# Kernel tuning notes

Measured on AMD Instinct MI355X. Metric: run time of the kernel, lower is better.

## Reference

```python
import jax, jax.numpy as jnp
import numpy as np

N = 16000        # nodes
E = 256000       # edges
D_IN = 1280      # input node features
HID = 256        # hidden dim (all hidden_dims equal; required by res_linear shapes)
HEADS = 8
C = HID // HEADS # 32 channels per head
G = 32           # graphs in the batch
O = 64           # output labels (GO terms)
NB = 2           # conv blocks = len(hidden_dims) - 1
EPS = 1e-5


def _bn(h, g, b):
    # eval-mode BatchNorm1d with running_mean=0, running_var=1 (init state)
    return h * (g / jnp.sqrt(1.0 + EPS)) + b


def _seg_softmax(logits, seg, num):
    # numerically-stable segment softmax (PyG softmax semantics)
    m = jax.ops.segment_max(logits, seg, num_segments=num)
    e = jnp.exp(logits - m[seg])
    s = jax.ops.segment_sum(e, seg, num_segments=num)
    return e / (s[seg] + 1e-16)


def setup_inputs() -> dict:
    key = jax.random.key(0)
    ks = jax.random.split(key, 16)
    w = lambda i, sh: jax.random.normal(ks[i], sh, jnp.float32) * 0.05
    return {
        "x": jax.random.normal(ks[0], (N, D_IN), jnp.float32),
        "edge_index": jax.random.randint(ks[1], (2, E), 0, N),
        "batch": jnp.sort(jax.random.randint(ks[2], (N,), 0, G)),
        # feature_proj: Linear -> ReLU -> BN
        "fp_W": w(3, (D_IN, HID)), "fp_b": jnp.zeros(HID),
        "fp_g": jnp.ones(HID), "fp_be": jnp.zeros(HID),
        # GATv2Conv per block: lin_l, lin_r, att, out-bias
        "gat_Wl": w(4, (NB, HID, HID)), "gat_bl": jnp.zeros((NB, HID)),
        "gat_Wr": w(5, (NB, HID, HID)), "gat_br": jnp.zeros((NB, HID)),
        "gat_att": w(6, (NB, HEADS, C)), "gat_bias": jnp.zeros((NB, HID)),
        # GINConv MLP: Linear -> ReLU -> BN
        "gin_W": w(7, (NB, HID, HID)), "gin_b": jnp.zeros((NB, HID)),
        "gin_g": jnp.ones((NB, HID)), "gin_be": jnp.zeros((NB, HID)),
        # PyG LayerNorm (graph mode) affine
        "ln_g": jnp.ones((NB, HID)), "ln_b": jnp.zeros((NB, HID)),
        # residual linears
        "res_W": w(8, (NB, HID, HID)), "res_b": jnp.zeros((NB, HID)),
        # GlobalAttention gate MLP
        "pool_W1": w(9, (HID, HID)), "pool_b1": jnp.zeros(HID),
        "pool_W2": w(10, (HID, 1)), "pool_b2": jnp.zeros(1),
        # O label heads (hierarchy=None -> just the MLP), stacked
        "head_W1": w(11, (O, HID, 256)), "head_b1": jnp.zeros((O, 256)),
        "head_g": jnp.ones((O, 256)), "head_be": jnp.zeros((O, 256)),
        "head_W2": w(12, (O, 256)), "head_b2": jnp.zeros(O),
    }


def reference(x, edge_index, batch, fp_W, fp_b, fp_g, fp_be,
              gat_Wl, gat_bl, gat_Wr, gat_br, gat_att, gat_bias,
              gin_W, gin_b, gin_g, gin_be, ln_g, ln_b, res_W, res_b,
              pool_W1, pool_b1, pool_W2, pool_b2,
              head_W1, head_b1, head_g, head_be, head_W2, head_b2):
    n = x.shape[0]
    # feature_proj (eval: dropout = identity)
    h = _bn(jax.nn.relu(x @ fp_W + fp_b), fp_g, fp_be)

    src0, dst0 = edge_index[0], edge_index[1]
    loop = jnp.arange(n)
    src = jnp.concatenate([src0, loop])  # GATv2 adds self-loops by default
    dst = jnp.concatenate([dst0, loop])

    for i in range(NB):
        # ---- GATv2Conv (no activation after, per original control flow) ----
        xl = (h @ gat_Wl[i] + gat_bl[i]).reshape(n, HEADS, C)
        xr = (h @ gat_Wr[i] + gat_br[i]).reshape(n, HEADS, C)
        msg = xl[src]                                   # [E', H, C]
        eact = jax.nn.leaky_relu(msg + xr[dst], 0.2)
        logit = jnp.einsum('ehc,hc->eh', eact, gat_att[i])
        alpha = _seg_softmax(logit, dst, n)             # [E', H]
        h = jax.ops.segment_sum(alpha[:, :, None] * msg, dst,
                                num_segments=n).reshape(n, HID) + gat_bias[i]
        # ---- GINConv: nn((1+0)*x + sum_neighbors), then leaky_relu ----
        agg = jax.ops.segment_sum(h[src0], dst0, num_segments=n)
        gin = _bn(jax.nn.relu((h + agg) @ gin_W[i] + gin_b[i]), gin_g[i], gin_be[i])
        h = jax.nn.leaky_relu(gin, 0.2)
        # ---- PyG LayerNorm (graph mode, batch=None: global mean/std) + residual ----
        mu = h.mean()
        sd = jnp.std(h)
        ln = (h - mu) / (sd + EPS) * ln_g[i] + ln_b[i]
        h = jax.nn.leaky_relu(ln + (h @ res_W[i] + res_b[i]), 0.2)

    # ---- GlobalAttention pooling ----
    gate = jnp.tanh(h @ pool_W1 + pool_b1) @ pool_W2 + pool_b2   # [N, 1]
    a = _seg_softmax(gate[:, 0], batch, G)
    emb = jax.ops.segment_sum(a[:, None] * h, batch, num_segments=G)  # [G, HID]

    # ---- O label heads (hierarchy None -> MLP only), vectorized ----
    z = jnp.einsum('bd,odh->boh', emb, head_W1) + head_b1[None]
    z = _bn(jax.nn.silu(z), head_g[None], head_be[None])
    out = jnp.einsum('boh,oh->bo', z, head_W2) + head_b2[None]
    return out[:, :, None]  # torch.stack(outputs, dim=1) -> [G, O, 1]
```

## Files before the change

### kernel.cpp

```cpp
#include <hip/hip_runtime.h>
#include <math.h>

#define N_NODES 16000
#define N_EDGES 256000
#define EPE (N_EDGES + N_NODES)
#define DIN 1280
#define HID 256
#define HEADS 8
#define CPH 32
#define NG 32
#define NO 64
#define EPSC 1e-5f
#define CAP 32
#define XPAD 264
#define SPAD 40

typedef __bf16 bf16;
typedef __attribute__((ext_vector_type(8))) __bf16 bf16x8;
typedef __attribute__((ext_vector_type(4))) float floatx4;

__device__ __forceinline__ float lrelu(float v) { return v > 0.f ? v : 0.2f * v; }
__device__ __forceinline__ float bflo(unsigned int u) { return __uint_as_float(u << 16); }
__device__ __forceinline__ float bfhi(unsigned int u) { return __uint_as_float(u & 0xffff0000u); }

__global__ void wconv_gen(const float* __restrict__ W, bf16* __restrict__ Wt, int K, int total) {
    int idx = blockIdx.x * 256 + threadIdx.x;
    if (idx >= total) return;
    int per = K * HID;
    int l = idx / per, rem = idx - l * per;
    int n = rem / K, k = rem - n * K;
    Wt[idx] = (bf16)W[(size_t)l * per + (size_t)k * HID + n];
}

__global__ void wconv_pair(const float* __restrict__ Wl, const float* __restrict__ Wr,
                           bf16* __restrict__ Wt) {
    int idx = blockIdx.x * 256 + threadIdx.x;
    int n = idx >> 8, k = idx & 255;
    float v = (n < 256) ? Wl[(size_t)k * HID + n] : Wr[(size_t)k * HID + (n - 256)];
    Wt[idx] = (bf16)v;
}

__global__ __launch_bounds__(256) void gemm64(
    const bf16* __restrict__ A, const bf16* __restrict__ Bt,
    const float* __restrict__ bias, const float* __restrict__ bias2,
    bf16* __restrict__ C, int K, int ldc, int mode,
    const float* __restrict__ g, const float* __restrict__ be)
{
    __shared__ __align__(16) bf16 As[2][64 * SPAD];
    __shared__ __align__(16) bf16 Bs[2][64 * SPAD];
    const int tid = threadIdx.x;
    const int bm = blockIdx.y * 64, bn = blockIdx.x * 64;
    const int w = tid >> 6, lane = tid & 63;
    const int wm = w * 16;
    const int lrow = lane & 15, lk8 = (lane >> 4) * 8;
    const int row = tid >> 2, k8 = (tid & 3) * 8;

    const bf16* gA = A + (size_t)(bm + row) * K + k8;
    const bf16* gB = Bt + (size_t)(bn + row) * K + k8;

    floatx4 acc[4];
#pragma unroll
    for (int j = 0; j < 4; j++) acc[j] = (floatx4){0.f, 0.f, 0.f, 0.f};

    const int nk = K >> 5;
    bf16x8 ra = *(const bf16x8*)gA;
    bf16x8 rb = *(const bf16x8*)gB;

    for (int it = 0; it < nk; ++it) {
        int p = it & 1;
        *(bf16x8*)&As[p][row * SPAD + k8] = ra;
        *(bf16x8*)&Bs[p][row * SPAD + k8] = rb;
        __syncthreads();
        if (it + 1 < nk) {
            ra = *(const bf16x8*)(gA + (it + 1) * 32);
            rb = *(const bf16x8*)(gB + (it + 1) * 32);
        }
        bf16x8 af = *(const bf16x8*)&As[p][(wm + lrow) * SPAD + lk8];
        bf16x8 bfr[4];
#pragma unroll
        for (int j = 0; j < 4; j++) bfr[j] = *(const bf16x8*)&Bs[p][(16 * j + lrow) * SPAD + lk8];
#pragma unroll
        for (int j = 0; j < 4; j++)
            acc[j] = __builtin_amdgcn_mfma_f32_16x16x32_bf16(af, bfr[j], acc[j], 0, 0, 0);
    }

    const float inv = rsqrtf(1.f + EPSC);
    const int row0 = bm + wm + (lane >> 4) * 4;
#pragma unroll
    for (int j = 0; j < 4; j++) {
        int col = bn + 16 * j + lrow;
        float bcol = (col < HID) ? bias[col] : bias2[col - HID];
        float gc = (mode >= 1) ? g[col] * inv : 0.f;
        float bec = (mode >= 1) ? be[col] : 0.f;
#pragma unroll
        for (int r = 0; r < 4; r++) {
            float z = acc[j][r] + bcol;
            if (mode >= 1) { z = fmaxf(z, 0.f); z = z * gc + bec; }
            if (mode == 2) z = lrelu(z);
            C[(size_t)(row0 + r) * ldc + col] = (bf16)z;
        }
    }
}

__global__ __launch_bounds__(256, 1) void gemm_f32A(
    const float* __restrict__ A, const bf16* __restrict__ Bt,
    const float* __restrict__ bias, bf16* __restrict__ C, int K,
    const float* __restrict__ g, const float* __restrict__ be)
{
    __shared__ __align__(16) bf16 As[2][128 * SPAD];
    __shared__ __align__(16) bf16 Bs[2][128 * SPAD];
    const int tid = threadIdx.x;
    const int bm = blockIdx.y * 128, bn = blockIdx.x * 128;
    const int w = tid >> 6, lane = tid & 63;
    const int wm = (w & 1) * 64, wn = (w >> 1) * 64;
    const int lrow = lane & 15, lk8 = (lane >> 4) * 8;

    floatx4 acc[4][4];
#pragma unroll
    for (int i = 0; i < 4; i++)
#pragma unroll
        for (int j = 0; j < 4; j++) acc[i][j] = (floatx4){0.f, 0.f, 0.f, 0.f};

    const int r2 = tid >> 1, c2 = tid & 1;
    const float* gA = A + (size_t)(bm + r2) * K + c2 * 16;
    const bf16* gB = Bt + (size_t)(bn + r2) * K + c2 * 16;
    bf16* sA = &As[0][r2 * SPAD + c2 * 16];
    bf16* sB = &Bs[0][r2 * SPAD + c2 * 16];

    const int nk = K >> 5;
    float4 a[4][4];
    bf16x8 b[4][2];
#pragma unroll
    for (int u = 0; u < 4; u++) {
        const float* pa = gA + u * 32;
        a[u][0] = *(const float4*)(pa + 0);
        a[u][1] = *(const float4*)(pa + 4);
        a[u][2] = *(const float4*)(pa + 8);
        a[u][3] = *(const float4*)(pa + 12);
        const bf16* pb = gB + u * 32;
        b[u][0] = *(const bf16x8*)(pb + 0);
        b[u][1] = *(const bf16x8*)(pb + 8);
    }

    for (int it0 = 0; it0 < nk; it0 += 4) {
#pragma unroll
        for (int u = 0; u < 4; u++) {
            const int it = it0 + u;
            const int p = u & 1;
            const int po = p * 128 * SPAD;
            bf16x8 h0, h1;
            h0[0] = (bf16)a[u][0].x; h0[1] = (bf16)a[u][0].y; h0[2] = (bf16)a[u][0].z; h0[3] = (bf16)a[u][0].w;
            h0[4] = (bf16)a[u][1].x; h0[5] = (bf16)a[u][1].y; h0[6] = (bf16)a[u][1].z; h0[7] = (bf16)a[u][1].w;
            h1[0] = (bf16)a[u][2].x; h1[1] = (bf16)a[u][2].y; h1[2] = (bf16)a[u][2].z; h1[3] = (bf16)a[u][2].w;
            h1[4] = (bf16)a[u][3].x; h1[5] = (bf16)a[u][3].y; h1[6] = (bf16)a[u][3].z; h1[7] = (bf16)a[u][3].w;
            *(bf16x8*)(sA + po + 0) = h0;
            *(bf16x8*)(sA + po + 8) = h1;
            *(bf16x8*)(sB + po + 0) = b[u][0];
            *(bf16x8*)(sB + po + 8) = b[u][1];
            __syncthreads();
            if (it + 4 < nk) {
                const float* pa = gA + (it + 4) * 32;
                a[u][0] = *(const float4*)(pa + 0);
                a[u][1] = *(const float4*)(pa + 4);
                a[u][2] = *(const float4*)(pa + 8);
                a[u][3] = *(const float4*)(pa + 12);
                const bf16* pb = gB + (it + 4) * 32;
                b[u][0] = *(const bf16x8*)(pb + 0);
                b[u][1] = *(const bf16x8*)(pb + 8);
            }
            bf16x8 af[4], bfr[4];
#pragma unroll
            for (int i = 0; i < 4; i++) af[i] = *(const bf16x8*)&As[p][(wm + 16 * i + lrow) * SPAD + lk8];
#pragma unroll
            for (int j = 0; j < 4; j++) bfr[j] = *(const bf16x8*)&Bs[p][(wn + 16 * j + lrow) * SPAD + lk8];
#pragma unroll
            for (int i = 0; i < 4; i++)
#pragma unroll
                for (int j = 0; j < 4; j++)
                    acc[i][j] = __builtin_amdgcn_mfma_f32_16x16x32_bf16(af[i], bfr[j], acc[i][j], 0, 0, 0);
        }
    }

    const float inv = rsqrtf(1.f + EPSC);
#pragma unroll
    for (int j = 0; j < 4; j++) {
        int col = bn + wn + 16 * j + lrow;
        float bcol = bias[col];
        float gc = g[col] * inv;
        float bec = be[col];
#pragma unroll
        for (int i = 0; i < 4; i++) {
            int row0 = bm + wm + 16 * i + (lane >> 4) * 4;
#pragma unroll
            for (int r = 0; r < 4; r++) {
                float z = fmaxf(acc[i][j][r] + bcol, 0.f) * gc + bec;
                C[(size_t)(row0 + r) * HID + col] = (bf16)z;
            }
        }
    }
}

__global__ void hist_kernel(const int* __restrict__ ei, int* __restrict__ cnt) {
    int e = blockIdx.x * 256 + threadIdx.x;
    if (e >= EPE) return;
    int d = (e < N_EDGES) ? ei[N_EDGES + e] : (e - N_EDGES);
    atomicAdd(&cnt[d], 1);
}

__global__ __launch_bounds__(1024) void scan_kernel(const int* __restrict__ cnt,
                                                    int* __restrict__ roff, int* __restrict__ cursor) {
    __shared__ int wsum[16];
    int t = threadIdx.x;
    int base = t * 16;
    int local[16]; int s = 0;
#pragma unroll
    for (int i = 0; i < 16; i++) {
        int idx = base + i;
        int v = (idx < N_NODES) ? cnt[idx] : 0;
        local[i] = s; s += v;
    }
    int lane = t & 63, wid = t >> 6;
    int incl = s;
    for (int o = 1; o < 64; o <<= 1) { int v = __shfl_up(incl, o); if (lane >= o) incl += v; }
    if (lane == 63) wsum[wid] = incl;
    __syncthreads();
    if (t == 0) { int a = 0; for (int k = 0; k < 16; k++) { int v = wsum[k]; wsum[k] = a; a += v; } }
    __syncthreads();
    int texcl = incl - s + wsum[wid];
#pragma unroll
    for (int i = 0; i < 16; i++) {
        int idx = base + i;
        if (idx < N_NODES) { int o = texcl + local[i]; roff[idx] = o; cursor[idx] = o; }
    }
    if (t == 1023) roff[N_NODES] = texcl + s;
}

__global__ void scatter_kernel(const int* __restrict__ ei, int* __restrict__ cursor,
                               int* __restrict__ esrc) {
    int e = blockIdx.x * 256 + threadIdx.x;
    if (e >= EPE) return;
    int s, d;
    if (e < N_EDGES) { s = ei[e]; d = ei[N_EDGES + e]; }
    else { s = d = e - N_EDGES; }
    int pos = atomicAdd(&cursor[d], 1);
    esrc[pos] = s;
}

__global__ __launch_bounds__(256) void gat_fused(
    const bf16* __restrict__ XLR, const int* __restrict__ roff, const int* __restrict__ esrc,
    const float* __restrict__ att, const float* __restrict__ gbias, bf16* __restrict__ out)
{
    const int d = blockIdx.x, t = threadIdx.x;
    const int beg = roff[d], deg = roff[d + 1] - beg;
    __shared__ __align__(16) bf16 xs[CAP][XPAD];
    __shared__ __align__(16) float4 xa4[8 * 16];
    __shared__ float llog[CAP * 8];
    __shared__ float m_s[8], s_s[8], resc[8];

    if (t < 128) {
        int hh = t >> 4, cc = t & 15;
        int c = hh * 32 + cc * 2;
        float xr0 = (float)XLR[(size_t)d * 512 + 256 + c];
        float xr1 = (float)XLR[(size_t)d * 512 + 256 + c + 1];
        xa4[hh * 16 + cc] = (float4){xr0, att[c], xr1, att[c + 1]};
    }
    if (t < 8) { m_s[t] = -INFINITY; s_s[t] = 0.f; }

    const int jj = t & 31;
    const int hh = t >> 5;
    const int g = t >> 5, l = t & 31;
    float acc = 0.f;

    for (int c0 = 0; c0 < deg; c0 += CAP) {
        int cn = min(CAP, deg - c0);
        __syncthreads();
        for (int r = g; r < cn; r += 8) {
            int s = esrc[beg + c0 + r];
            *(bf16x8*)(&xs[r][l * 8]) = *(const bf16x8*)(XLR + (size_t)s * 512 + l * 8);
        }
        __syncthreads();
        if (jj < cn) {
            float lg = 0.f;
#pragma unroll
            for (int cc = 0; cc < 16; cc++) {
                int ce = (cc + jj) & 15;
                unsigned int p = *(const unsigned int*)&xs[jj][hh * 32 + ce * 2];
                float4 xa = xa4[hh * 16 + ce];
                lg += lrelu(bflo(p) + xa.x) * xa.y + lrelu(bfhi(p) + xa.z) * xa.w;
            }
            llog[jj * 8 + hh] = lg;
        }
        __syncthreads();
        if (t < 64) {
            int h2 = t & 7, j0 = t >> 3;
            float mx = -INFINITY;
            for (int j = j0; j < cn; j += 8) mx = fmaxf(mx, llog[j * 8 + h2]);
            for (int o = 8; o < 64; o <<= 1) mx = fmaxf(mx, __shfl_xor(mx, o));
            float mo = m_s[h2];
            float mn = fmaxf(mo, mx);
            float ss = 0.f;
            for (int j = j0; j < cn; j += 8) {
                float e = __expf(llog[j * 8 + h2] - mn);
                llog[j * 8 + h2] = e;
                ss += e;
            }
            for (int o = 8; o < 64; o <<= 1) ss += __shfl_xor(ss, o);
            if (t < 8) {
                float r = __expf(mo - mn);
                resc[h2] = r;
                s_s[h2] = s_s[h2] * r + ss;
                m_s[h2] = mn;
            }
        }
        __syncthreads();
        acc *= resc[hh];
        for (int j = 0; j < cn; j++)
            acc += llog[j * 8 + hh] * (float)xs[j][t];
    }
    out[(size_t)d * HID + t] = (bf16)(gbias[t] + acc / (s_s[hh] + 1e-16f));
}

__global__ __launch_bounds__(256) void gin_gather(
    const unsigned int* __restrict__ hu, const int* __restrict__ roff,
    const int* __restrict__ esrc, unsigned int* __restrict__ uu)
{
    int d = blockIdx.x, t = threadIdx.x;
    int grp = t >> 7, c = t & 127;
    int beg = roff[d], end = roff[d + 1];
    float a0 = 0.f, a1 = 0.f;
    int p = beg + grp;
    while (p + 14 < end) {
        int s[8];
#pragma unroll
        for (int k = 0; k < 8; k++) s[k] = esrc[p + 2 * k];
        unsigned int v[8];
#pragma unroll
        for (int k = 0; k < 8; k++) v[k] = hu[(size_t)s[k] * 128 + c];
#pragma unroll
        for (int k = 0; k < 8; k++) { a0 += bflo(v[k]); a1 += bfhi(v[k]); }
        p += 16;
    }
    for (; p < end; p += 2) {
        unsigned int v = hu[(size_t)esrc[p] * 128 + c];
        a0 += bflo(v); a1 += bfhi(v);
    }
    __shared__ float plo[128], phi[128];
    if (grp) { plo[c] = a0; phi[c] = a1; }
    __syncthreads();
    if (!grp) {
        a0 += plo[c]; a1 += phi[c];
        bf16 b0 = (bf16)a0, b1 = (bf16)a1;
        unsigned int r = ((unsigned int)*(unsigned short*)&b0) |
                         (((unsigned int)*(unsigned short*)&b1) << 16);
        uu[(size_t)d * 128 + c] = r;
    }
}

__global__ void stats_kernel(const bf16* __restrict__ x, float2* __restrict__ part, int n8) {
    float s = 0.f, sq = 0.f;
    for (int i = blockIdx.x * blockDim.x + threadIdx.x; i < n8; i += gridDim.x * blockDim.x) {
        bf16x8 v = *(const bf16x8*)(x + (size_t)i * 8);
#pragma unroll
        for (int j = 0; j < 8; j++) { float f = (float)v[j]; s += f; sq += f * f; }
    }
    for (int o = 32; o > 0; o >>= 1) { s += __shfl_down(s, o); sq += __shfl_down(sq, o); }
    __shared__ float ls[4], lq[4];
    int wid = threadIdx.x >> 6, lane = threadIdx.x & 63;
    if (lane == 0) { ls[wid] = s; lq[wid] = sq; }
    __syncthreads();
    if (threadIdx.x == 0)
        part[blockIdx.x] = make_float2(ls[0] + ls[1] + ls[2] + ls[3],
                                       lq[0] + lq[1] + lq[2] + lq[3]);
}

__global__ void stats_reduce(const float2* __restrict__ part, float* __restrict__ stat) {
    int t = threadIdx.x;
    float2 v = part[t];
    float s = v.x, q = v.y;
    for (int o = 32; o > 0; o >>= 1) { s += __shfl_down(s, o); q += __shfl_down(q, o); }
    __shared__ float ls[4], lq[4];
    int wid = t >> 6, lane = t & 63;
    if (lane == 0) { ls[wid] = s; lq[wid] = q; }
    __syncthreads();
    if (t == 0) { stat[0] = ls[0] + ls[1] + ls[2] + ls[3]; stat[1] = lq[0] + lq[1] + lq[2] + lq[3]; }
}

__global__ void ln_res_kernel(const bf16* __restrict__ h, const bf16* __restrict__ r,
                              const float* __restrict__ stats, const float* __restrict__ g,
                              const float* __restrict__ b, bf16* __restrict__ out)
{
    int i = (blockIdx.x * 256 + threadIdx.x) * 4;
    const float inv_n = 1.f / (float)((size_t)N_NODES * HID);
    float mu = stats[0] * inv_n;
    float var = stats[1] * inv_n - mu * mu;
    float sd = sqrtf(fmaxf(var, 0.f));
    float rs = 1.f / (sd + EPSC);
    int ch = i & (HID - 1);
#pragma unroll
    for (int j = 0; j < 4; j++) {
        float v = ((float)h[i + j] - mu) * rs * g[ch + j] + b[ch + j] + (float)r[i + j];
        out[i + j] = (bf16)lrelu(v);
    }
}

__global__ void gbound_kernel(const int* __restrict__ batch, int* __restrict__ gstart) {
    int g = threadIdx.x;
    if (g > NG) return;
    int lo = 0, hi = N_NODES;
    while (lo < hi) { int mid = (lo + hi) >> 1; if (batch[mid] < g) lo = mid + 1; else hi = mid; }
    gstart[g] = lo;
}

__global__ __launch_bounds__(256) void pool_gate_kernel(const bf16* __restrict__ t,
    const float* __restrict__ W2, const float* __restrict__ b2, float* __restrict__ gate)
{
    int n = blockIdx.x * 4 + (threadIdx.x >> 6);
    int lane = threadIdx.x & 63;
    const bf16* p = t + (size_t)n * HID + lane * 4;
    float4 w = *(const float4*)(W2 + lane * 4);
    float s = tanhf((float)p[0]) * w.x + tanhf((float)p[1]) * w.y
            + tanhf((float)p[2]) * w.z + tanhf((float)p[3]) * w.w;
    for (int o = 32; o > 0; o >>= 1) s += __shfl_down(s, o);
    if (lane == 0) gate[n] = s + b2[0];
}

__global__ __launch_bounds__(256) void pool_stats_kernel(
    float* __restrict__ gate, const int* __restrict__ gstart)
{
    int g = blockIdx.x, t = threadIdx.x;
    int lo = gstart[g], hi = gstart[g + 1];
    __shared__ float red[256];
    float m = -INFINITY;
    for (int n = lo + t; n < hi; n += 256) m = fmaxf(m, gate[n]);
    red[t] = m; __syncthreads();
    for (int st = 128; st > 0; st >>= 1) { if (t < st) red[t] = fmaxf(red[t], red[t + st]); __syncthreads(); }
    m = red[0]; __syncthreads();
    float s = 0.f;
    for (int n = lo + t; n < hi; n += 256) s += __expf(gate[n] - m);
    red[t] = s; __syncthreads();
    for (int st = 128; st > 0; st >>= 1) { if (t < st) red[t] += red[t + st]; __syncthreads(); }
    float sinv = 1.f / (red[0] + 1e-16f);
    for (int n = lo + t; n < hi; n += 256) gate[n] = __expf(gate[n] - m) * sinv;
}

__global__ __launch_bounds__(256) void emb_accum_kernel(
    const float* __restrict__ a, const int* __restrict__ batch,
    const bf16* __restrict__ h, float* __restrict__ emb)
{
    int n0 = blockIdx.x * 32, t = threadIdx.x;
    int cur = batch[n0]; float acc = 0.f;
    for (int j = 0; j < 32; j++) {
        int n = n0 + j;
        int b = batch[n];
        if (b != cur) { atomicAdd(&emb[cur * HID + t], acc); cur = b; acc = 0.f; }
        acc += a[n] * (float)h[(size_t)n * HID + t];
    }
    atomicAdd(&emb[cur * HID + t], acc);
}

__global__ __launch_bounds__(256) void heads_kernel(
    const float* __restrict__ emb, const float* __restrict__ W1, const float* __restrict__ b1,
    const float* __restrict__ hg, const float* __restrict__ hbe, const float* __restrict__ W2,
    const float* __restrict__ b2, float* __restrict__ out)
{
    int o = blockIdx.x;
    int g0 = blockIdx.y * 4;
    int k = threadIdx.x;
    __shared__ float se[4][HID];
    __shared__ float red[256];
#pragma unroll
    for (int j = 0; j < 4; j++) se[j][k] = emb[(g0 + j) * HID + k];
    __syncthreads();
    const float* w1p = W1 + (size_t)o * HID * HID + k;
    float zb = b1[o * HID + k];
    float z0 = zb, z1 = zb, z2 = zb, z3 = zb;
#pragma unroll 8
    for (int d = 0; d < HID; d++) {
        float w = w1p[(size_t)d * HID];
        z0 = fmaf(se[0][d], w, z0);
        z1 = fmaf(se[1][d], w, z1);
        z2 = fmaf(se[2][d], w, z2);
        z3 = fmaf(se[3][d], w, z3);
    }
    const float gk = hg[o * HID + k] * rsqrtf(1.f + EPSC);
    const float bek = hbe[o * HID + k];
    const float w2 = W2[o * HID + k];
    const float b2o = b2[o];
    float zz[4] = {z0, z1, z2, z3};
#pragma unroll
    for (int j = 0; j < 4; j++) {
        float z = zz[j];
        float sil = z / (1.f + expf(-z));
        red[k] = (sil * gk + bek) * w2;
        __syncthreads();
        for (int st = 128; st > 0; st >>= 1) { if (k < st) red[k] += red[k + st]; __syncthreads(); }
        if (k == 0) out[(g0 + j) * NO + o] = red[0] + b2o;
        __syncthreads();
    }
}

extern "C" void kernel_launch(void* const* d_in, const int* in_sizes, int n_in,
                              void* d_out, int out_size, void* d_ws, size_t ws_size,
                              hipStream_t stream) {
    const float* x        = (const float*)d_in[0];
    const int*   ei       = (const int*)  d_in[1];
    const int*   batch    = (const int*)  d_in[2];
    const float* fp_W     = (const float*)d_in[3];
    const float* fp_b     = (const float*)d_in[4];
    const float* fp_g     = (const float*)d_in[5];
    const float* fp_be    = (const float*)d_in[6];
    const float* gat_Wl   = (const float*)d_in[7];
    const float* gat_bl   = (const float*)d_in[8];
    const float* gat_Wr   = (const float*)d_in[9];
    const float* gat_br   = (const float*)d_in[10];
    const float* gat_att  = (const float*)d_in[11];
    const float* gat_bias = (const float*)d_in[12];
    const float* gin_W    = (const float*)d_in[13];
    const float* gin_b    = (const float*)d_in[14];
    const float* gin_g    = (const float*)d_in[15];
    const float* gin_be   = (const float*)d_in[16];
    const float* ln_g     = (const float*)d_in[17];
    const float* ln_b     = (const float*)d_in[18];
    const float* res_W    = (const float*)d_in[19];
    const float* res_b    = (const float*)d_in[20];
    const float* pool_W1  = (const float*)d_in[21];
    const float* pool_b1  = (const float*)d_in[22];
    const float* pool_W2  = (const float*)d_in[23];
    const float* pool_b2  = (const float*)d_in[24];
    const float* head_W1  = (const float*)d_in[25];
    const float* head_b1  = (const float*)d_in[26];
    const float* head_g   = (const float*)d_in[27];
    const float* head_be  = (const float*)d_in[28];
    const float* head_W2  = (const float*)d_in[29];
    const float* head_b2  = (const float*)d_in[30];
    float* out = (float*)d_out;

    char* base = (char*)d_ws;
    size_t off = 0;
    auto alloc = [&](size_t bytes) -> char* {
        char* p = base + off; off += (bytes + 255) & ~(size_t)255; return p;
    };
    int*   esrc   = (int*)  alloc((size_t)EPE * 4);
    int*   cnt    = (int*)  alloc((size_t)N_NODES * 4);
    int*   roff   = (int*)  alloc((size_t)(N_NODES + 1) * 4);
    int*   cursor = (int*)  alloc((size_t)N_NODES * 4);
    float* gate   = (float*)alloc((size_t)N_NODES * 4);
    int*   gstart = (int*)  alloc((NG + 1) * 4);
    float* emb    = (float*)alloc(NG * HID * 4);
    float* stat   = (float*)alloc(8);
    float2* statp = (float2*)alloc(256 * 8);
    bf16*  Hb0    = (bf16*) alloc((size_t)N_NODES * HID * 2);
    bf16*  Hb1    = (bf16*) alloc((size_t)N_NODES * HID * 2);
    bf16*  XLR    = (bf16*) alloc((size_t)N_NODES * 512 * 2);
    bf16*  fpWt   = (bf16*) alloc((size_t)DIN * HID * 2);
    bf16*  wlrT0  = (bf16*) alloc((size_t)512 * HID * 2);
    bf16*  wlrT1  = (bf16*) alloc((size_t)512 * HID * 2);
    bf16*  gwT    = (bf16*) alloc((size_t)2 * HID * HID * 2);
    bf16*  rwT    = (bf16*) alloc((size_t)2 * HID * HID * 2);
    bf16*  pwT    = (bf16*) alloc((size_t)HID * HID * 2);
    bf16*  Ub     = XLR;
    bf16*  wlrT[2] = { wlrT0, wlrT1 };

    wconv_gen<<<(DIN * HID + 255) / 256, 256, 0, stream>>>(fp_W, fpWt, DIN, DIN * HID);
    wconv_pair<<<512, 256, 0, stream>>>(gat_Wl, gat_Wr, wlrT0);
    wconv_pair<<<512, 256, 0, stream>>>(gat_Wl + HID * HID, gat_Wr + HID * HID, wlrT1);
    wconv_gen<<<512, 256, 0, stream>>>(gin_W, gwT, HID, 2 * HID * HID);
    wconv_gen<<<512, 256, 0, stream>>>(res_W, rwT, HID, 2 * HID * HID);
    wconv_gen<<<256, 256, 0, stream>>>(pool_W1, pwT, HID, HID * HID);

    hipMemsetAsync(cnt, 0, N_NODES * sizeof(int), stream);
    hist_kernel<<<(EPE + 255) / 256, 256, 0, stream>>>(ei, cnt);
    scan_kernel<<<1, 1024, 0, stream>>>(cnt, roff, cursor);
    scatter_kernel<<<(EPE + 255) / 256, 256, 0, stream>>>(ei, cursor, esrc);
    gbound_kernel<<<1, 64, 0, stream>>>(batch, gstart);

    dim3 gridF(2, 125);
    dim3 g64_256(4, 250);
    dim3 g64_512(8, 250);
    gemm_f32A<<<gridF, 256, 0, stream>>>(x, fpWt, fp_b, Hb0, DIN, fp_g, fp_be);

    for (int i = 0; i < 2; i++) {
        gemm64<<<g64_512, 256, 0, stream>>>(Hb0, wlrT[i], gat_bl + i * HID, gat_br + i * HID,
                                            XLR, HID, 512, 0, nullptr, nullptr);
        gat_fused<<<N_NODES, 256, 0, stream>>>(XLR, roff, esrc, gat_att + i * HEADS * CPH,
                                               gat_bias + i * HID, Hb1);
        gin_gather<<<N_NODES, 256, 0, stream>>>((const unsigned int*)Hb1, roff, esrc,
                                                (unsigned int*)Ub);
        gemm64<<<g64_256, 256, 0, stream>>>(Ub, gwT + (size_t)i * HID * HID, gin_b + i * HID,
                                            nullptr, Hb0, HID, HID, 2,
                                            gin_g + i * HID, gin_be + i * HID);
        stats_kernel<<<256, 256, 0, stream>>>(Hb0, statp, (N_NODES * HID) / 8);
        stats_reduce<<<1, 256, 0, stream>>>(statp, stat);
        gemm64<<<g64_256, 256, 0, stream>>>(Hb0, rwT + (size_t)i * HID * HID, res_b + i * HID,
                                            nullptr, Hb1, HID, HID, 0, nullptr, nullptr);
        ln_res_kernel<<<(N_NODES * HID) / 1024, 256, 0, stream>>>(Hb0, Hb1, stat,
                                                                  ln_g + i * HID, ln_b + i * HID, Hb0);
    }

    gemm64<<<g64_256, 256, 0, stream>>>(Hb0, pwT, pool_b1, nullptr, Hb1, HID, HID, 0, nullptr, nullptr);
    pool_gate_kernel<<<N_NODES / 4, 256, 0, stream>>>(Hb1, pool_W2, pool_b2, gate);
    pool_stats_kernel<<<NG, 256, 0, stream>>>(gate, gstart);
    hipMemsetAsync(emb, 0, NG * HID * sizeof(float), stream);
    emb_accum_kernel<<<N_NODES / 32, 256, 0, stream>>>(gate, batch, Hb0, emb);

    dim3 hgrid(NO, 8);
    heads_kernel<<<hgrid, 256, 0, stream>>>(emb, head_W1, head_b1, head_g, head_be,
                                            head_W2, head_b2, out);
}
```

Measured before the change: 608.4 us.

## Merge weight conversions, fold graph bounds into scan, fuse pooling, split GAT aggregation

The six weight-conversion launches become one kernel, and the graph-boundary search moves into the scan kernel. The pooling softmax and embedding accumulation are fused into one per-graph kernel, which removes the memset and the atomics. In the GAT kernel, each thread now handles two channels and the two halves of the block split the edges and combine through shared memory, using packed bf16 stores. This cuts launch overhead and atomics, but the pooling now runs on only 32 blocks, each looping serially over roughly 500 nodes, which may reduce parallelism.

```diff
diff --git a/kernel.cpp b/kernel.cpp
--- a/kernel.cpp
+++ b/kernel.cpp
@@ -22,22 +22,44 @@
 __device__ __forceinline__ float lrelu(float v) { return v > 0.f ? v : 0.2f * v; }
 __device__ __forceinline__ float bflo(unsigned int u) { return __uint_as_float(u << 16); }
 __device__ __forceinline__ float bfhi(unsigned int u) { return __uint_as_float(u & 0xffff0000u); }
-
-__global__ void wconv_gen(const float* __restrict__ W, bf16* __restrict__ Wt, int K, int total) {
+__device__ __forceinline__ unsigned int bfpack(float x, float y) {
+    bf16 b0 = (bf16)x, b1 = (bf16)y;
+    return ((unsigned int)*(unsigned short*)&b0) | (((unsigned int)*(unsigned short*)&b1) << 16);
+}
+
+__global__ void wconv_all(const float* __restrict__ fp_W, const float* __restrict__ Wl,
+                          const float* __restrict__ Wr, const float* __restrict__ gin_W,
+                          const float* __restrict__ res_W, const float* __restrict__ pool_W1,
+                          bf16* __restrict__ fpWt, bf16* __restrict__ wlrT0,
+                          bf16* __restrict__ wlrT1, bf16* __restrict__ gwT,
+                          bf16* __restrict__ rwT, bf16* __restrict__ pwT)
+{
     int idx = blockIdx.x * 256 + threadIdx.x;
-    if (idx >= total) return;
-    int per = K * HID;
-    int l = idx / per, rem = idx - l * per;
-    int n = rem / K, k = rem - n * K;
-    Wt[idx] = (bf16)W[(size_t)l * per + (size_t)k * HID + n];
-}
-
-__global__ void wconv_pair(const float* __restrict__ Wl, const float* __restrict__ Wr,
-                           bf16* __restrict__ Wt) {
-    int idx = blockIdx.x * 256 + threadIdx.x;
-    int n = idx >> 8, k = idx & 255;
-    float v = (n < 256) ? Wl[(size_t)k * HID + n] : Wr[(size_t)k * HID + (n - 256)];
-    Wt[idx] = (bf16)v;
+    if (idx < 327680) {
+        int n = idx / DIN, k = idx - n * DIN;
+        fpWt[idx] = (bf16)fp_W[(size_t)k * HID + n];
+    } else if (idx < 327680 + 262144) {
+        int r = idx - 327680;
+        int layer = r >> 17, rr = r & 131071;
+        int n = rr >> 8, k = rr & 255;
+        const float* Ws = (n < 256) ? (Wl + layer * 65536) : (Wr + layer * 65536);
+        bf16 v = (bf16)Ws[k * HID + (n & 255)];
+        if (layer) wlrT1[rr] = v; else wlrT0[rr] = v;
+    } else if (idx < 327680 + 262144 + 131072) {
+        int r = idx - (327680 + 262144);
+        int l = r >> 16, nk = r & 65535;
+        int n = nk >> 8, k = nk & 255;
+        gwT[r] = (bf16)gin_W[(l << 16) + (k << 8) + n];
+    } else if (idx < 327680 + 262144 + 262144) {
+        int r = idx - (327680 + 262144 + 131072);
+        int l = r >> 16, nk = r & 65535;
+        int n = nk >> 8, k = nk & 255;
+        rwT[r] = (bf16)res_W[(l << 16) + (k << 8) + n];
+    } else if (idx < 327680 + 262144 + 262144 + 65536) {
+        int r = idx - (327680 + 262144 + 262144);
+        int n = r >> 8, k = r & 255;
+        pwT[r] = (bf16)pool_W1[(k << 8) + n];
+    }
 }
 
 __global__ __launch_bounds__(256) void gemm64(
@@ -208,7 +230,9 @@
 }
 
 __global__ __launch_bounds__(1024) void scan_kernel(const int* __restrict__ cnt,
-                                                    int* __restrict__ roff, int* __restrict__ cursor) {
+                                                    int* __restrict__ roff, int* __restrict__ cursor,
+                                                    const int* __restrict__ batch,
+                                                    int* __restrict__ gstart) {
     __shared__ int wsum[16];
     int t = threadIdx.x;
     int base = t * 16;
@@ -233,6 +257,11 @@
         if (idx < N_NODES) { int o = texcl + local[i]; roff[idx] = o; cursor[idx] = o; }
     }
     if (t == 1023) roff[N_NODES] = texcl + s;
+    if (t <= NG) {
+        int lo = 0, hi = N_NODES;
+        while (lo < hi) { int mid = (lo + hi) >> 1; if (batch[mid] < t) lo = mid + 1; else hi = mid; }
+        gstart[t] = lo;
+    }
 }
 
 __global__ void scatter_kernel(const int* __restrict__ ei, int* __restrict__ cursor,
@@ -255,6 +284,7 @@
     __shared__ __align__(16) bf16 xs[CAP][XPAD];
     __shared__ __align__(16) float4 xa4[8 * 16];
     __shared__ float llog[CAP * 8];
+    __shared__ float comb[256];
     __shared__ float m_s[8], s_s[8], resc[8];
 
     if (t < 128) {
@@ -268,15 +298,19 @@
 
     const int jj = t & 31;
     const int hh = t >> 5;
-    const int g = t >> 5, l = t & 31;
-    float acc = 0.f;
+    const int sg = t >> 5, sl = t & 31;
+    const int half = t >> 7;
+    const int tc = t & 127;
+    const int ch0 = tc * 2;
+    const int ha = tc >> 4;
+    float a0 = 0.f, a1 = 0.f;
 
     for (int c0 = 0; c0 < deg; c0 += CAP) {
         int cn = min(CAP, deg - c0);
         __syncthreads();
-        for (int r = g; r < cn; r += 8) {
+        for (int r = sg; r < cn; r += 8) {
             int s = esrc[beg + c0 + r];
-            *(bf16x8*)(&xs[r][l * 8]) = *(const bf16x8*)(XLR + (size_t)s * 512 + l * 8);
+            *(bf16x8*)(&xs[r][sl * 8]) = *(const bf16x8*)(XLR + (size_t)s * 512 + sl * 8);
         }
         __syncthreads();
         if (jj < cn) {
@@ -313,11 +347,24 @@
             }
         }
         __syncthreads();
-        acc *= resc[hh];
-        for (int j = 0; j < cn; j++)
-            acc += llog[j * 8 + hh] * (float)xs[j][t];
-    }
-    out[(size_t)d * HID + t] = (bf16)(gbias[t] + acc / (s_s[hh] + 1e-16f));
+        float rs = resc[ha];
+        a0 *= rs; a1 *= rs;
+        for (int j = half; j < cn; j += 2) {
+            float wgt = llog[j * 8 + ha];
+            unsigned int p = *(const unsigned int*)&xs[j][ch0];
+            a0 = fmaf(wgt, bflo(p), a0);
+            a1 = fmaf(wgt, bfhi(p), a1);
+        }
+    }
+    __syncthreads();
+    if (half) { comb[ch0] = a0; comb[ch0 + 1] = a1; }
+    __syncthreads();
+    if (!half) {
+        float r = 1.f / (s_s[ha] + 1e-16f);
+        float v0 = gbias[ch0] + (a0 + comb[ch0]) * r;
+        float v1 = gbias[ch0 + 1] + (a1 + comb[ch0 + 1]) * r;
+        *(unsigned int*)(out + (size_t)d * HID + ch0) = bfpack(v0, v1);
+    }
 }
 
 __global__ __launch_bounds__(256) void gin_gather(
@@ -349,10 +396,7 @@
     __syncthreads();
     if (!grp) {
         a0 += plo[c]; a1 += phi[c];
-        bf16 b0 = (bf16)a0, b1 = (bf16)a1;
-        unsigned int r = ((unsigned int)*(unsigned short*)&b0) |
-                         (((unsigned int)*(unsigned short*)&b1) << 16);
-        uu[(size_t)d * 128 + c] = r;
+        uu[(size_t)d * 128 + c] = bfpack(a0, a1);
     }
 }
 
@@ -403,14 +447,6 @@
     }
 }
 
-__global__ void gbound_kernel(const int* __restrict__ batch, int* __restrict__ gstart) {
-    int g = threadIdx.x;
-    if (g > NG) return;
-    int lo = 0, hi = N_NODES;
-    while (lo < hi) { int mid = (lo + hi) >> 1; if (batch[mid] < g) lo = mid + 1; else hi = mid; }
-    gstart[g] = lo;
-}
-
 __global__ __launch_bounds__(256) void pool_gate_kernel(const bf16* __restrict__ t,
     const float* __restrict__ W2, const float* __restrict__ b2, float* __restrict__ gate)
 {
@@ -424,38 +460,36 @@
     if (lane == 0) gate[n] = s + b2[0];
 }
 
-__global__ __launch_bounds__(256) void pool_stats_kernel(
-    float* __restrict__ gate, const int* __restrict__ gstart)
+__global__ __launch_bounds__(256) void pool_emb_kernel(
+    const float* __restrict__ gate, const int* __restrict__ gstart,
+    const bf16* __restrict__ h, float* __restrict__ emb)
 {
     int g = blockIdx.x, t = threadIdx.x;
     int lo = gstart[g], hi = gstart[g + 1];
+    int cnt = hi - lo;
     __shared__ float red[256];
+    __shared__ float alpha[1024];
     float m = -INFINITY;
     for (int n = lo + t; n < hi; n += 256) m = fmaxf(m, gate[n]);
     red[t] = m; __syncthreads();
     for (int st = 128; st > 0; st >>= 1) { if (t < st) red[t] = fmaxf(red[t], red[t + st]); __syncthreads(); }
     m = red[0]; __syncthreads();
     float s = 0.f;
-    for (int n = lo + t; n < hi; n += 256) s += __expf(gate[n] - m);
+    for (int n = lo + t; n < hi; n += 256) {
+        float e = __expf(gate[n] - m);
+        if (n - lo < 1024) alpha[n - lo] = e;
+        s += e;
+    }
     red[t] = s; __syncthreads();
     for (int st = 128; st > 0; st >>= 1) { if (t < st) red[t] += red[t + st]; __syncthreads(); }
     float sinv = 1.f / (red[0] + 1e-16f);
-    for (int n = lo + t; n < hi; n += 256) gate[n] = __expf(gate[n] - m) * sinv;
-}
-
-__global__ __launch_bounds__(256) void emb_accum_kernel(
-    const float* __restrict__ a, const int* __restrict__ batch,
-    const bf16* __restrict__ h, float* __restrict__ emb)
-{
-    int n0 = blockIdx.x * 32, t = threadIdx.x;
-    int cur = batch[n0]; float acc = 0.f;
-    for (int j = 0; j < 32; j++) {
-        int n = n0 + j;
-        int b = batch[n];
-        if (b != cur) { atomicAdd(&emb[cur * HID + t], acc); cur = b; acc = 0.f; }
-        acc += a[n] * (float)h[(size_t)n * HID + t];
-    }
-    atomicAdd(&emb[cur * HID + t], acc);
+    float acc = 0.f;
+    const bf16* hp = h + (size_t)lo * HID + t;
+    for (int n = 0; n < cnt; n++) {
+        float a = (n < 1024) ? alpha[n] : __expf(gate[lo + n] - m);
+        acc += a * (float)hp[(size_t)n * HID];
+    }
+    emb[g * HID + t] = acc * sinv;
 }
 
 __global__ __launch_bounds__(256) void heads_kernel(
@@ -561,18 +595,13 @@
     bf16*  Ub     = XLR;
     bf16*  wlrT[2] = { wlrT0, wlrT1 };
 
-    wconv_gen<<<(DIN * HID + 255) / 256, 256, 0, stream>>>(fp_W, fpWt, DIN, DIN * HID);
-    wconv_pair<<<512, 256, 0, stream>>>(gat_Wl, gat_Wr, wlrT0);
-    wconv_pair<<<512, 256, 0, stream>>>(gat_Wl + HID * HID, gat_Wr + HID * HID, wlrT1);
-    wconv_gen<<<512, 256, 0, stream>>>(gin_W, gwT, HID, 2 * HID * HID);
-    wconv_gen<<<512, 256, 0, stream>>>(res_W, rwT, HID, 2 * HID * HID);
-    wconv_gen<<<256, 256, 0, stream>>>(pool_W1, pwT, HID, HID * HID);
+    wconv_all<<<3584, 256, 0, stream>>>(fp_W, gat_Wl, gat_Wr, gin_W, res_W, pool_W1,
+                                        fpWt, wlrT0, wlrT1, gwT, rwT, pwT);
 
     hipMemsetAsync(cnt, 0, N_NODES * sizeof(int), stream);
     hist_kernel<<<(EPE + 255) / 256, 256, 0, stream>>>(ei, cnt);
-    scan_kernel<<<1, 1024, 0, stream>>>(cnt, roff, cursor);
+    scan_kernel<<<1, 1024, 0, stream>>>(cnt, roff, cursor, batch, gstart);
     scatter_kernel<<<(EPE + 255) / 256, 256, 0, stream>>>(ei, cursor, esrc);
-    gbound_kernel<<<1, 64, 0, stream>>>(batch, gstart);
 
     dim3 gridF(2, 125);
     dim3 g64_256(4, 250);
@@ -599,9 +628,7 @@
 
     gemm64<<<g64_256, 256, 0, stream>>>(Hb0, pwT, pool_b1, nullptr, Hb1, HID, HID, 0, nullptr, nullptr);
     pool_gate_kernel<<<N_NODES / 4, 256, 0, stream>>>(Hb1, pool_W2, pool_b2, gate);
-    pool_stats_kernel<<<NG, 256, 0, stream>>>(gate, gstart);
-    hipMemsetAsync(emb, 0, NG * HID * sizeof(float), stream);
-    emb_accum_kernel<<<N_NODES / 32, 256, 0, stream>>>(gate, batch, Hb0, emb);
+    pool_emb_kernel<<<NG, 256, 0, stream>>>(gate, gstart, Hb0, emb);
 
     dim3 hgrid(NO, 8);
     heads_kernel<<<hgrid, 256, 0, stream>>>(emb, head_W1, head_b1, head_g, head_be,
```

Result: slower. 633.9 us (+4.2%).
